# Performance work log

Hardware: AMD Instinct MI355X
Metric: run time of the kernel (lower is better)

The kernel has to match this reference:

```python
import jax, jax.numpy as jnp
import numpy as np

MAX_LEN, BATCH, EMB = 512, 32, 41
HID, UNITS = 800, 20
BOND_LENS = jnp.array([1.329, 1.459, 1.525], jnp.float32)
BOND_ANGLES = jnp.array([2.034, 2.119, 1.937], jnp.float32)
INIT_ABC = jnp.array([[0.0, 0.0, 1.0], [0.0, 1.0, 0.0], [1.0, 0.0, 0.0]], jnp.float32)


def _lstm_dir(x, w_ih, w_hh, b, reverse):
    # x: [T, B, in]; returns hidden states [T, B, H]
    T, B, _ = x.shape
    H = w_hh.shape[1]
    xs = jnp.flip(x, 0) if reverse else x
    xw = jnp.einsum('tbi,gi->tbg', xs, w_ih) + b  # precompute input projection

    def step(carry, xt):
        h, c = carry
        gates = xt + h @ w_hh.T
        i, f, g, o = jnp.split(gates, 4, axis=-1)
        c = jax.nn.sigmoid(f) * c + jax.nn.sigmoid(i) * jnp.tanh(g)
        h = jax.nn.sigmoid(o) * jnp.tanh(c)
        return (h, c), h

    init = (jnp.zeros((B, H), x.dtype), jnp.zeros((B, H), x.dtype))
    _, hs = jax.lax.scan(step, init, xw)
    return jnp.flip(hs, 0) if reverse else hs


def _bilstm_layer(x, w_ih, w_hh, b):
    # w_ih: [2, 4H, in]; w_hh: [2, 4H, H]; b: [2, 4H]
    fwd = _lstm_dir(x, w_ih[0], w_hh[0], b[0], False)
    bwd = _lstm_dir(x, w_ih[1], w_hh[1], b[1], True)
    return jnp.concatenate([fwd, bwd], axis=-1)


def _geometric_unit(coords3, triplet):
    # coords3: [3, B, 3] last three atoms; triplet: [B, 3] torsion angles
    A, Bc, C = coords3[0], coords3[1], coords3[2]
    new = []
    for i in range(3):
        Tang, R, P = BOND_ANGLES[i], BOND_LENS[i], triplet[:, i]
        D2 = jnp.stack([-R * jnp.cos(Tang) * jnp.ones_like(P),
                        R * jnp.cos(P) * jnp.sin(Tang),
                        R * jnp.sin(P) * jnp.sin(Tang)], axis=1)  # [B,3]
        BC = C - Bc
        bc = BC / jnp.linalg.norm(BC, axis=1, keepdims=True)
        AB = Bc - A
        N = jnp.cross(AB, bc)
        n = N / jnp.linalg.norm(N, axis=1, keepdims=True)
        M = jnp.stack([bc, jnp.cross(n, bc), n], axis=2)  # [B,3,3]
        D = jnp.einsum('bij,bj->bi', M, D2) + C
        A, Bc, C = Bc, C, D
        new.append(D)
    return jnp.stack([A, Bc, C]), jnp.stack(new)  # carry, [3,B,3]


def setup_inputs() -> dict:
    key = jax.random.key(0)
    ks = jax.random.split(key, 10)
    k = 1.0 / np.sqrt(HID)
    u = lambda kk, shp, lim: jax.random.uniform(kk, shp, jnp.float32, -lim, lim)
    in0, in1 = EMB + 1, 2 * HID
    return {
        'sequences': jax.random.normal(ks[0], (MAX_LEN, BATCH, EMB), jnp.float32),
        'lengths': jnp.full((BATCH,), MAX_LEN, jnp.int64 if jax.config.jax_enable_x64 else jnp.int32),
        'w_ih0': u(ks[1], (2, 4 * HID, in0), k),
        'w_hh0': u(ks[2], (2, 4 * HID, HID), k),
        'b0': u(ks[3], (2, 4 * HID), k),
        'w_ih1': u(ks[4], (2, 4 * HID, in1), k),
        'w_hh1': u(ks[5], (2, 4 * HID, HID), k),
        'b1': u(ks[6], (2, 4 * HID), k),
        'lin_w': u(ks[7], (UNITS, 2 * HID), 1.0 / np.sqrt(2 * HID)),
        'lin_b': u(ks[8], (UNITS,), 1.0 / np.sqrt(2 * HID)),
        'alphabet': jax.random.uniform(ks[9], (UNITS, 3), jnp.float32, -3.14, 3.14),
    }


def reference(sequences, lengths, w_ih0, w_hh0, b0, w_ih1, w_hh1, b1, lin_w, lin_b, alphabet):
    T, B, _ = sequences.shape
    abs_pos = jnp.broadcast_to(jnp.arange(T, dtype=sequences.dtype)[:, None, None], (T, B, 1))
    x = jnp.concatenate([sequences, abs_pos], axis=2)  # [T, B, EMB+1]
    # 2-layer bidirectional LSTM (all lengths == max_len -> packing is identity)
    h = _bilstm_layer(x, w_ih0, w_hh0, b0)
    h = _bilstm_layer(h, w_ih1, w_hh1, b1)  # [T, B, 2H]
    # linear -> softmax over alphabet, trig angle decode
    soft = jax.nn.softmax(h @ lin_w.T + lin_b, axis=2)  # [T, B, UNITS]
    sine = soft @ jnp.sin(alphabet)   # [T, B, 3]
    cosine = soft @ jnp.cos(alphabet)
    out = jnp.arctan2(sine, cosine)   # torsion angle triplets
    # sequential geometric coordinate recurrence over timesteps 1..T-1
    init = jnp.broadcast_to(INIT_ABC[:, None, :], (3, B, 3))
    _, new_coords = jax.lax.scan(_geometric_unit, init, out[1:])  # [T-1, 3, B, 3]
    pred_coords = jnp.concatenate([init, new_coords.reshape(-1, B, 3)], axis=0)
    return pred_coords  # [3 + 3*(T-1), B, 3]
```

## Files before the change

### kernel.cpp

```cpp
#include <hip/hip_runtime.h>
#include <math.h>

#define T_LEN 512
#define NB    32
#define EMB_  41
#define IN0_  42
#define HID_  800
#define G4_   3200
#define IN1_  1600
#define NU    20
#define NCH   100

typedef unsigned short u16;
typedef unsigned int   u32;
typedef unsigned long long u64;
typedef __attribute__((ext_vector_type(8))) short short8;
typedef __attribute__((ext_vector_type(4))) float f32x4;

__device__ __forceinline__ float bf2f(u16 v) {
    union { u32 u; float f; } c; c.u = ((u32)v) << 16; return c.f;
}
__device__ __forceinline__ u16 f2bf(float f) {
    union { float f; u32 u; } c; c.f = f;
    u32 r = (c.u + 0x7fffu + ((c.u >> 16) & 1u)) >> 16;
    return (u16)r;
}
__device__ __forceinline__ short cvt_hl(float v, int hl) {
    u16 hi = f2bf(v);
    return hl ? (short)f2bf(v - bf2f(hi)) : (short)hi;
}
__device__ __forceinline__ f32x4 mfma16(short8 a, short8 b, f32x4 c) {
    return __builtin_amdgcn_mfma_f32_16x16x32_bf16(a, b, c, 0, 0, 0);
}
__device__ __forceinline__ void astore(u64* p, u64 v) {
    __hip_atomic_store(p, v, __ATOMIC_RELAXED, __HIP_MEMORY_SCOPE_AGENT);
}
__device__ __forceinline__ int afload(const int* p) {
    return __hip_atomic_load(p, __ATOMIC_RELAXED, __HIP_MEMORY_SCOPE_AGENT);
}
__device__ __forceinline__ void afstore(int* p, int v) {
    __hip_atomic_store(p, v, __ATOMIC_RELAXED, __HIP_MEMORY_SCOPE_AGENT);
}


__global__ __launch_bounds__(256, 1)
void lstm0_persist(const float* __restrict__ seq, const float* __restrict__ wih0,
                   const float* __restrict__ whh0, const float* __restrict__ bias,
                   u16* __restrict__ h0f, int* __restrict__ flags)
{
    __shared__ __align__(16) float part[2048];
    __shared__ __align__(16) u16 stageB[25600];
    __shared__ __align__(16) float w0l[32*48];
    __shared__ __align__(16) float xsl[32*48];
    __shared__ u16 hpk[NB*8];
    const int tid = threadIdx.x;
    const int d = blockIdx.x / NCH, ch = blockIdx.x % NCH;
    const int w = tid >> 6, l = tid & 63;
    const int p = w & 1, hl = w >> 1;
    int* myflags = flags + d*128;

    short8 wreg[25];
    {
        const int m = l & 15, g = p*2 + (m>>3), j = ch*8 + (m&7);
        const float* base = whh0 + ((size_t)(d*G4_ + g*HID_ + j))*HID_ + (l>>4)*8;
#pragma unroll
        for (int kc = 0; kc < 25; ++kc) {
            float4 f0 = *(const float4*)(base + kc*32);
            float4 f1 = *(const float4*)(base + kc*32 + 4);
            short8 v;
            v[0]=cvt_hl(f0.x,hl); v[1]=cvt_hl(f0.y,hl); v[2]=cvt_hl(f0.z,hl); v[3]=cvt_hl(f0.w,hl);
            v[4]=cvt_hl(f1.x,hl); v[5]=cvt_hl(f1.y,hl); v[6]=cvt_hl(f1.z,hl); v[7]=cvt_hl(f1.w,hl);
            wreg[kc] = v;
        }
    }
    for (int idx = tid; idx < 32*EMB_; idx += 256) {
        int r = idx / EMB_, k = idx % EMB_;
        int ju_ = r >> 2, g = r & 3;
        w0l[r*48 + k] = wih0[((size_t)(d*G4_ + g*HID_ + ch*8 + ju_))*IN0_ + k];
    }
    const int ju = tid >> 5, b = tid & 31;
    const int j = ch*8 + ju;
    const int nt = b >> 4, n = b & 15;
    float biasr[4], wpos[4];
#pragma unroll
    for (int g = 0; g < 4; ++g) {
        biasr[g] = bias[d*G4_ + g*HID_ + j];
        wpos[g]  = wih0[((size_t)(d*G4_ + g*HID_ + j))*IN0_ + EMB_];
    }
    float creg = 0.f;
    __syncthreads();

    for (int s = 0; s < T_LEN; ++s) {
        const int t = d ? (T_LEN-1-s) : s;

        for (int idx = tid; idx < 32*EMB_; idx += 256)
            xsl[(idx/EMB_)*48 + idx%EMB_] = seq[(size_t)t*(NB*EMB_) + idx];

        if (s > 0 && tid < NCH)
            while (afload(myflags + tid) < s) __builtin_amdgcn_s_sleep(1);
        __syncthreads();

        if (s == 0) {
#pragma unroll
            for (int q = 0; q < 25; ++q) ((u64*)stageB)[tid + q*256] = 0ull;
        } else {
            const int tprev = d ? (T_LEN - s) : (s - 1);
            const u64* src = (const u64*)(h0f + (size_t)tprev*51200) + d*6400;
            u64 tmp[25];
#pragma unroll
            for (int q = 0; q < 25; ++q) tmp[q] = src[tid + q*256];
#pragma unroll
            for (int q = 0; q < 25; ++q) ((u64*)stageB)[tid + q*256] = tmp[q];
        }
        __syncthreads();

        f32x4 acc0 = {0.f,0.f,0.f,0.f}, acc1 = {0.f,0.f,0.f,0.f};
#pragma unroll 5
        for (int kc = 0; kc < 25; ++kc) {
            short8 b0 = *(const short8*)(stageB + kc*1024 + l*8);
            short8 b1 = *(const short8*)(stageB + kc*1024 + 512 + l*8);
            acc0 = mfma16(wreg[kc], b0, acc0);
            acc1 = mfma16(wreg[kc], b1, acc1);
        }
        {
            const int mrow = (l>>4)*4, nn = l & 15;
#pragma unroll
            for (int r = 0; r < 4; ++r) {
                part[(((p*2+hl)*2 + 0)*16 + mrow + r)*16 + nn] = acc0[r];
                part[(((p*2+hl)*2 + 1)*16 + mrow + r)*16 + nn] = acc1[r];
            }
        }
        __syncthreads();

        float dot0 = 0.f, dot1 = 0.f, dot2 = 0.f, dot3 = 0.f;
        {
            const float* wr = &w0l[ju*4*48];
            const float* xr = &xsl[b*48];
#pragma unroll
            for (int k4 = 0; k4 < 40; k4 += 4) {
                float4 xk = *(const float4*)(xr + k4);
                float4 w0 = *(const float4*)(wr + 0*48 + k4);
                float4 w1 = *(const float4*)(wr + 1*48 + k4);
                float4 w2 = *(const float4*)(wr + 2*48 + k4);
                float4 w3 = *(const float4*)(wr + 3*48 + k4);
                dot0 += w0.x*xk.x + w0.y*xk.y + w0.z*xk.z + w0.w*xk.w;
                dot1 += w1.x*xk.x + w1.y*xk.y + w1.z*xk.z + w1.w*xk.w;
                dot2 += w2.x*xk.x + w2.y*xk.y + w2.z*xk.z + w2.w*xk.w;
                dot3 += w3.x*xk.x + w3.y*xk.y + w3.z*xk.z + w3.w*xk.w;
            }
            float xk = xr[40];
            dot0 += wr[0*48+40]*xk; dot1 += wr[1*48+40]*xk;
            dot2 += wr[2*48+40]*xk; dot3 += wr[3*48+40]*xk;
        }
        float v[4] = {dot0, dot1, dot2, dot3};
#pragma unroll
        for (int g = 0; g < 4; ++g) {
            const int pp = g >> 1, m = (g & 1)*8 + ju;
            v[g] += part[(((pp*2+0)*2 + nt)*16 + m)*16 + n]
                  + part[(((pp*2+1)*2 + nt)*16 + m)*16 + n]
                  + biasr[g] + (float)t * wpos[g];
        }
        float ig = 1.f/(1.f + expf(-v[0]));
        float fg = 1.f/(1.f + expf(-v[1]));
        float gg = tanhf(v[2]);
        float og = 1.f/(1.f + expf(-v[3]));
        creg = fg * creg + ig * gg;
        hpk[b*8 + ju] = f2bf(og * tanhf(creg));
        __syncthreads();

        if (tid < 64) {
            const int bb = tid >> 1, half = tid & 1;
            const u16* hp = &hpk[bb*8 + half*4];
            u64 pk = (u64)hp[0] | ((u64)hp[1]<<16) | ((u64)hp[2]<<32) | ((u64)hp[3]<<48);
            const int ntb = bb >> 4, llb = ((ch&3)<<4) | (bb&15);
            const int xoff = ((d*25 + (ch>>2))*2 + ntb)*128 + llb*2 + half;
            astore((u64*)(h0f + (size_t)t*51200) + xoff, pk);
        }
        __syncthreads();
        if (tid == 0) afstore(myflags + ch, s+1);
    }
}

__global__ __launch_bounds__(256, 1)
void lstm1_persist(const float* __restrict__ wih1, const float* __restrict__ whh1,
                   const float* __restrict__ bias, const float* __restrict__ lin_w,
                   const u16* __restrict__ h0f, u16* __restrict__ h1f,
                   int* __restrict__ flags, float* __restrict__ logits)
{
    __shared__ __align__(16) u16 wihL[2*50*512];
    __shared__ __align__(16) u16 stageB[25600];
    __shared__ __align__(16) float part[2048];
    __shared__ u16 hpk[NB*8];
    const int tid = threadIdx.x;
    const int d = blockIdx.x / NCH, ch = blockIdx.x % NCH;
    const int w = tid >> 6, l = tid & 63;
    const int p = w & 1, hl = w >> 1;
    int* myflags = flags + d*128;

    short8 wreg[25];
    {
        const int m = l & 15, g = p*2 + (m>>3), j = ch*8 + (m&7);
        const float* base = whh1 + ((size_t)(d*G4_ + g*HID_ + j))*HID_ + (l>>4)*8;
#pragma unroll
        for (int kc = 0; kc < 25; ++kc) {
            float4 f0 = *(const float4*)(base + kc*32);
            float4 f1 = *(const float4*)(base + kc*32 + 4);
            short8 v;
            v[0]=cvt_hl(f0.x,hl); v[1]=cvt_hl(f0.y,hl); v[2]=cvt_hl(f0.z,hl); v[3]=cvt_hl(f0.w,hl);
            v[4]=cvt_hl(f1.x,hl); v[5]=cvt_hl(f1.y,hl); v[6]=cvt_hl(f1.z,hl); v[7]=cvt_hl(f1.w,hl);
            wreg[kc] = v;
        }
    }
    for (int o = tid; o < 6400; o += 256) {
        int pp = o / 3200, r = o % 3200, kc = r >> 6, ll = r & 63;
        int m = ll & 15, g = pp*2 + (m>>3), jj = ch*8 + (m&7);
        const float* base = wih1 + ((size_t)(d*G4_ + g*HID_ + jj))*IN1_ + kc*32 + (ll>>4)*8;
        float4 f0 = *(const float4*)base;
        float4 f1 = *(const float4*)(base + 4);
        short8 v;
        v[0]=(short)f2bf(f0.x); v[1]=(short)f2bf(f0.y); v[2]=(short)f2bf(f0.z); v[3]=(short)f2bf(f0.w);
        v[4]=(short)f2bf(f1.x); v[5]=(short)f2bf(f1.y); v[6]=(short)f2bf(f1.z); v[7]=(short)f2bf(f1.w);
        *(short8*)&wihL[o*8] = v;
    }
    const int ol = tid >> 5, ln = tid & 31;
    const int lo = ch*7 + ol;
    const bool lown = (ol < 7) && (lo < NB*NU);
    int lofs = 0;
    float wlin[25];
    if (lown) {
        const int bb = lo / NU, uu = lo % NU;
        lofs = (bb >> 4)*512 + ((((ln >> 3) << 4) | (bb & 15)))*8 + (ln & 7);
        const float* wrow = lin_w + (size_t)uu*IN1_ + d*HID_ + ln;
#pragma unroll
        for (int i = 0; i < 25; ++i) wlin[i] = wrow[i*32];
    }
    const int ju = tid >> 5, b = tid & 31;
    const int j = ch*8 + ju;
    const int nt = b >> 4, n = b & 15;
    float biasr[4];
#pragma unroll
    for (int g = 0; g < 4; ++g) biasr[g] = bias[d*G4_ + g*HID_ + j];
    float creg = 0.f;
    __syncthreads();

    for (int s = 0; s < T_LEN; ++s) {
        const int t = d ? (T_LEN-1-s) : s;

        f32x4 acc0 = {0.f,0.f,0.f,0.f}, acc1 = {0.f,0.f,0.f,0.f};
        {
            const u16* xb = h0f + (size_t)t*51200;
#pragma unroll 5
            for (int kc = 0; kc < 25; ++kc) {
                const int idx = hl*25 + kc;
                short8 a  = *(const short8*)&wihL[(p*50 + idx)*512 + l*8];
                short8 b0 = *(const short8*)(xb + idx*1024 + l*8);
                short8 b1 = *(const short8*)(xb + idx*1024 + 512 + l*8);
                acc0 = mfma16(a, b0, acc0);
                acc1 = mfma16(a, b1, acc1);
            }
        }

        if (s > 0 && tid < NCH)
            while (afload(myflags + tid) < s) __builtin_amdgcn_s_sleep(1);
        __syncthreads();

        if (s == 0) {
#pragma unroll
            for (int q = 0; q < 25; ++q) ((u64*)stageB)[tid + q*256] = 0ull;
        } else {
            const int tprev = d ? (T_LEN - s) : (s - 1);
            const u64* src = (const u64*)(h1f + (size_t)tprev*51200) + d*6400;
            u64 tmp[25];
#pragma unroll
            for (int q = 0; q < 25; ++q) tmp[q] = src[tid + q*256];
#pragma unroll
            for (int q = 0; q < 25; ++q) ((u64*)stageB)[tid + q*256] = tmp[q];
        }
        __syncthreads();

#pragma unroll 5
        for (int kc = 0; kc < 25; ++kc) {
            short8 b0 = *(const short8*)(stageB + kc*1024 + l*8);
            short8 b1 = *(const short8*)(stageB + kc*1024 + 512 + l*8);
            acc0 = mfma16(wreg[kc], b0, acc0);
            acc1 = mfma16(wreg[kc], b1, acc1);
        }
        {
            const int mrow = (l>>4)*4, nn = l & 15;
#pragma unroll
            for (int r = 0; r < 4; ++r) {
                part[(((p*2+hl)*2 + 0)*16 + mrow + r)*16 + nn] = acc0[r];
                part[(((p*2+hl)*2 + 1)*16 + mrow + r)*16 + nn] = acc1[r];
            }
        }
        __syncthreads();

        float v[4];
#pragma unroll
        for (int g = 0; g < 4; ++g) {
            const int pp = g >> 1, m = (g & 1)*8 + ju;
            v[g] = part[(((pp*2+0)*2 + nt)*16 + m)*16 + n]
                 + part[(((pp*2+1)*2 + nt)*16 + m)*16 + n] + biasr[g];
        }
        float ig = 1.f/(1.f + expf(-v[0]));
        float fg = 1.f/(1.f + expf(-v[1]));
        float gg = tanhf(v[2]);
        float og = 1.f/(1.f + expf(-v[3]));
        creg = fg * creg + ig * gg;
        float hn = og * tanhf(creg);
        hpk[b*8 + ju] = f2bf(hn);
        __syncthreads();

        if (tid < 64) {
            const int bb = tid >> 1, half = tid & 1;
            const u16* hp = &hpk[bb*8 + half*4];
            u64 pk = (u64)hp[0] | ((u64)hp[1]<<16) | ((u64)hp[2]<<32) | ((u64)hp[3]<<48);
            const int ntb = bb >> 4, llb = ((ch&3)<<4) | (bb&15);
            const int xoff = ((d*25 + (ch>>2))*2 + ntb)*128 + llb*2 + half;
            astore((u64*)(h1f + (size_t)t*51200) + xoff, pk);
        }
        __syncthreads();
        if (tid == 0) afstore(myflags + ch, s+1);

        if (s > 0 && lown) {
            float sum = 0.f;
#pragma unroll
            for (int i = 0; i < 25; ++i)
                sum += bf2f(stageB[i*1024 + lofs]) * wlin[i];
#pragma unroll
            for (int off2 = 16; off2; off2 >>= 1) sum += __shfl_down(sum, off2, 32);
            if (ln == 0) {
                const int tprev = d ? (T_LEN - s) : (s - 1);
                logits[((size_t)d*T_LEN + tprev)*640 + lo] = sum;
            }
        }
    }
    if (tid < NCH)
        while (afload(myflags + tid) < T_LEN) __builtin_amdgcn_s_sleep(1);
    __syncthreads();
    {
        const int tlast = d ? 0 : (T_LEN - 1);
        const u64* src = (const u64*)(h1f + (size_t)tlast*51200) + d*6400;
        u64 tmp[25];
#pragma unroll
        for (int q = 0; q < 25; ++q) tmp[q] = src[tid + q*256];
#pragma unroll
        for (int q = 0; q < 25; ++q) ((u64*)stageB)[tid + q*256] = tmp[q];
    }
    __syncthreads();
    if (lown) {
        float sum = 0.f;
#pragma unroll
        for (int i = 0; i < 25; ++i)
            sum += bf2f(stageB[i*1024 + lofs]) * wlin[i];
#pragma unroll
        for (int off2 = 16; off2; off2 >>= 1) sum += __shfl_down(sum, off2, 32);
        if (ln == 0) {
            const int tprev = d ? 0 : (T_LEN - 1);
            logits[((size_t)d*T_LEN + tprev)*640 + lo] = sum;
        }
    }
}

__global__ __launch_bounds__(256)
void epilogue(const float* __restrict__ logits, const float* __restrict__ lin_b,
              const float* __restrict__ alphabet, float* __restrict__ cs)
{
    __shared__ float sa[NU*3], ca[NU*3], lb[NU];
    const int tid = threadIdx.x;
    if (tid < NU*3) { float al = alphabet[tid]; sa[tid] = sinf(al); ca[tid] = cosf(al); }
    if (tid < NU) lb[tid] = lin_b[tid];
    __syncthreads();
    const int row = blockIdx.x*256 + tid;
    if (row >= T_LEN*NB) return;
    const int t = row >> 5, b = row & 31;
    float lg[NU];
    float m = -1e30f;
#pragma unroll 4
    for (int u = 0; u < NU; ++u) {
        lg[u] = lb[u] + logits[(size_t)t*640 + b*NU + u]
                      + logits[((size_t)T_LEN + t)*640 + b*NU + u];
        m = fmaxf(m, lg[u]);
    }
    float ssum = 0.f;
#pragma unroll 4
    for (int u = 0; u < NU; ++u) { lg[u] = expf(lg[u] - m); ssum += lg[u]; }
    float inv = 1.f / ssum;
#pragma unroll
    for (int i = 0; i < 3; ++i) {
        float sv = 0.f, cv = 0.f;
#pragma unroll 4
        for (int u = 0; u < NU; ++u) {
            float sw = lg[u] * inv;
            sv += sw * sa[u*3 + i];
            cv += sw * ca[u*3 + i];
        }
        float rinv = rsqrtf(fmaxf(sv*sv + cv*cv, 1e-30f));
        *(float2*)(cs + ((size_t)row*3 + i)*2) = make_float2(cv*rinv, sv*rinv);
    }
}

__global__ __launch_bounds__(64)
void geometry(const float* __restrict__ cs, float* __restrict__ out)
{
    const int b = threadIdx.x;
    if (b >= NB) return;
    const float blen[3] = {1.329f, 1.459f, 1.525f};
    const float bang[3] = {2.034f, 2.119f, 1.937f};
    float sT[3], cT[3];
#pragma unroll
    for (int i = 0; i < 3; ++i) { sT[i] = sinf(bang[i]); cT[i] = cosf(bang[i]); }

    float Ax=0.f,Ay=0.f,Az=1.f, Bx=0.f,By=1.f,Bz=0.f, Cx=1.f,Cy=0.f,Cz=0.f;
    out[(0*NB + b)*3 + 0] = 0.f; out[(0*NB + b)*3 + 1] = 0.f; out[(0*NB + b)*3 + 2] = 1.f;
    out[(1*NB + b)*3 + 0] = 0.f; out[(1*NB + b)*3 + 1] = 1.f; out[(1*NB + b)*3 + 2] = 0.f;
    out[(2*NB + b)*3 + 0] = 1.f; out[(2*NB + b)*3 + 1] = 0.f; out[(2*NB + b)*3 + 2] = 0.f;

    for (int t = 1; t < T_LEN; ++t) {
        float2 pc[3];
#pragma unroll
        for (int i = 0; i < 3; ++i)
            pc[i] = *(const float2*)(cs + (((size_t)t*NB + b)*3 + i)*2);
#pragma unroll
        for (int i = 0; i < 3; ++i) {
            float R = blen[i];
            float d2x = -R*cT[i], d2y = R*pc[i].x*sT[i], d2z = R*pc[i].y*sT[i];
            float bcx = Cx-Bx, bcy = Cy-By, bcz = Cz-Bz;
            float inv = rsqrtf(bcx*bcx + bcy*bcy + bcz*bcz);
            bcx *= inv; bcy *= inv; bcz *= inv;
            float abx = Bx-Ax, aby = By-Ay, abz = Bz-Az;
            float nx = aby*bcz - abz*bcy;
            float ny = abz*bcx - abx*bcz;
            float nz = abx*bcy - aby*bcx;
            inv = rsqrtf(fmaxf(nx*nx + ny*ny + nz*nz, 1e-30f));
            nx *= inv; ny *= inv; nz *= inv;
            float mx = ny*bcz - nz*bcy;
            float my = nz*bcx - nx*bcz;
            float mz = nx*bcy - ny*bcx;
            float Dx = bcx*d2x + mx*d2y + nx*d2z + Cx;
            float Dy = bcy*d2x + my*d2y + ny*d2z + Cy;
            float Dz = bcz*d2x + mz*d2y + nz*d2z + Cz;
            Ax=Bx; Ay=By; Az=Bz; Bx=Cx; By=Cy; Bz=Cz; Cx=Dx; Cy=Dy; Cz=Dz;
            const int r = 3 + (t-1)*3 + i;
            out[((size_t)r*NB + b)*3 + 0] = Dx;
            out[((size_t)r*NB + b)*3 + 1] = Dy;
            out[((size_t)r*NB + b)*3 + 2] = Dz;
        }
    }
}

extern "C" void kernel_launch(void* const* d_in, const int* in_sizes, int n_in,
                              void* d_out, int out_size, void* d_ws, size_t ws_size,
                              hipStream_t stream)
{
    (void)in_sizes; (void)n_in; (void)out_size; (void)ws_size;
    const float* seq   = (const float*)d_in[0];
    const float* w_ih0 = (const float*)d_in[2];
    const float* w_hh0 = (const float*)d_in[3];
    const float* b0    = (const float*)d_in[4];
    const float* w_ih1 = (const float*)d_in[5];
    const float* w_hh1 = (const float*)d_in[6];
    const float* b1    = (const float*)d_in[7];
    const float* lin_w = (const float*)d_in[8];
    const float* lin_b = (const float*)d_in[9];
    const float* alpha = (const float*)d_in[10];

    char* ws = (char*)d_ws;
    size_t off = 0;
    u16* h0f   = (u16*)(ws + off); off += 52428800ull;
    u16* h1f   = (u16*)(ws + off); off += 52428800ull;
    int* flagsL0 = (int*)(ws + off); off += 1024ull;
    int* flagsL1 = (int*)(ws + off); off += 1024ull;
    float* logits = (float*)(ws + off); off += 2621440ull;
    float* cs = (float*)(ws + off); off += 393216ull;

    hipMemsetAsync(flagsL0, 0, 2048, stream);

    lstm0_persist<<<dim3(2*NCH), dim3(256), 0, stream>>>(seq, w_ih0, w_hh0, b0, h0f, flagsL0);

    lstm1_persist<<<dim3(2*NCH), dim3(256), 0, stream>>>(w_ih1, w_hh1, b1, lin_w, h0f, h1f,
                                                         flagsL1, logits);

    epilogue<<<dim3(64), dim3(256), 0, stream>>>(logits, lin_b, alpha, cs);
    geometry<<<dim3(1), dim3(64), 0, stream>>>(cs, (float*)d_out);
}
```

Before: 9.387 ms.

## Replace per-block flag polling with per-step arrival counters and per-wave stores

Each persistent LSTM kernel now has every wave atomically increment a per-timestep arrival counter after writing its own bf16 hidden values, and all threads spin on that single counter reaching 400. This replaces the earlier scheme of 100 threads polling 100 per-block flags, and it removes the LDS staging of h and two block-wide barriers per step. The x staging buffer is double-buffered so the barrier before the wait can be dropped, and the layer-1 logit projection now reads h from global memory instead of LDS. The risks are heavier atomic traffic on one hot counter address, and memory-ordering correctness that depends on relaxed atomics plus an explicit vmcnt wait.

```diff
diff --git a/kernel.cpp b/kernel.cpp
--- a/kernel.cpp
+++ b/kernel.cpp
@@ -10,6 +10,7 @@
 #define IN1_  1600
 #define NU    20
 #define NCH   100
+#define ARR_TGT (4*NCH)
 
 typedef unsigned short u16;
 typedef unsigned int   u32;
@@ -32,32 +33,31 @@
 __device__ __forceinline__ f32x4 mfma16(short8 a, short8 b, f32x4 c) {
     return __builtin_amdgcn_mfma_f32_16x16x32_bf16(a, b, c, 0, 0, 0);
 }
-__device__ __forceinline__ void astore(u64* p, u64 v) {
+__device__ __forceinline__ void astore32(u32* p, u32 v) {
     __hip_atomic_store(p, v, __ATOMIC_RELAXED, __HIP_MEMORY_SCOPE_AGENT);
 }
 __device__ __forceinline__ int afload(const int* p) {
     return __hip_atomic_load(p, __ATOMIC_RELAXED, __HIP_MEMORY_SCOPE_AGENT);
 }
-__device__ __forceinline__ void afstore(int* p, int v) {
-    __hip_atomic_store(p, v, __ATOMIC_RELAXED, __HIP_MEMORY_SCOPE_AGENT);
+__device__ __forceinline__ void aadd(int* p) {
+    __hip_atomic_fetch_add(p, 1, __ATOMIC_RELAXED, __HIP_MEMORY_SCOPE_AGENT);
 }
 
 
 __global__ __launch_bounds__(256, 1)
 void lstm0_persist(const float* __restrict__ seq, const float* __restrict__ wih0,
                    const float* __restrict__ whh0, const float* __restrict__ bias,
-                   u16* __restrict__ h0f, int* __restrict__ flags)
+                   u16* __restrict__ h0f, int* __restrict__ arr)
 {
     __shared__ __align__(16) float part[2048];
     __shared__ __align__(16) u16 stageB[25600];
     __shared__ __align__(16) float w0l[32*48];
-    __shared__ __align__(16) float xsl[32*48];
-    __shared__ u16 hpk[NB*8];
+    __shared__ __align__(16) float xsl[2][32*48];
     const int tid = threadIdx.x;
     const int d = blockIdx.x / NCH, ch = blockIdx.x % NCH;
     const int w = tid >> 6, l = tid & 63;
     const int p = w & 1, hl = w >> 1;
-    int* myflags = flags + d*128;
+    int* myarr = arr + d*512;
 
     short8 wreg[25];
     {
@@ -94,11 +94,10 @@
         const int t = d ? (T_LEN-1-s) : s;
 
         for (int idx = tid; idx < 32*EMB_; idx += 256)
-            xsl[(idx/EMB_)*48 + idx%EMB_] = seq[(size_t)t*(NB*EMB_) + idx];
-
-        if (s > 0 && tid < NCH)
-            while (afload(myflags + tid) < s) __builtin_amdgcn_s_sleep(1);
-        __syncthreads();
+            xsl[s&1][(idx/EMB_)*48 + idx%EMB_] = seq[(size_t)t*(NB*EMB_) + idx];
+
+        if (s > 0)
+            while (afload(myarr + (s-1)) < ARR_TGT) __builtin_amdgcn_s_sleep(1);
 
         if (s == 0) {
 #pragma unroll
@@ -135,7 +134,7 @@
         float dot0 = 0.f, dot1 = 0.f, dot2 = 0.f, dot3 = 0.f;
         {
             const float* wr = &w0l[ju*4*48];
-            const float* xr = &xsl[b*48];
+            const float* xr = &xsl[s&1][b*48];
 #pragma unroll
             for (int k4 = 0; k4 < 40; k4 += 4) {
                 float4 xk = *(const float4*)(xr + k4);
@@ -165,19 +164,18 @@
         float gg = tanhf(v[2]);
         float og = 1.f/(1.f + expf(-v[3]));
         creg = fg * creg + ig * gg;
-        hpk[b*8 + ju] = f2bf(og * tanhf(creg));
-        __syncthreads();
-
-        if (tid < 64) {
-            const int bb = tid >> 1, half = tid & 1;
-            const u16* hp = &hpk[bb*8 + half*4];
-            u64 pk = (u64)hp[0] | ((u64)hp[1]<<16) | ((u64)hp[2]<<32) | ((u64)hp[3]<<48);
-            const int ntb = bb >> 4, llb = ((ch&3)<<4) | (bb&15);
-            const int xoff = ((d*25 + (ch>>2))*2 + ntb)*128 + llb*2 + half;
-            astore((u64*)(h0f + (size_t)t*51200) + xoff, pk);
-        }
-        __syncthreads();
-        if (tid == 0) afstore(myflags + ch, s+1);
+        float hval = og * tanhf(creg);
+
+        u32 hv = (u32)f2bf(hval);
+        u32 ov = (u32)__shfl((int)hv, l | 32);
+        if (l < 32) {
+            const int ntb = b >> 4, llb = ((ch&3)<<4) | (b&15);
+            const int half = w >> 1;
+            const u32 xoff = (u32)(((d*25 + (ch>>2))*2 + ntb)*128 + llb*2 + half);
+            astore32((u32*)(h0f + (size_t)t*51200) + xoff*2 + (w&1), hv | (ov<<16));
+        }
+        asm volatile("s_waitcnt vmcnt(0)" ::: "memory");
+        if (l == 0) aadd(myarr + s);
     }
 }
 
@@ -185,17 +183,16 @@
 void lstm1_persist(const float* __restrict__ wih1, const float* __restrict__ whh1,
                    const float* __restrict__ bias, const float* __restrict__ lin_w,
                    const u16* __restrict__ h0f, u16* __restrict__ h1f,
-                   int* __restrict__ flags, float* __restrict__ logits)
+                   int* __restrict__ arr, float* __restrict__ logits)
 {
     __shared__ __align__(16) u16 wihL[2*50*512];
     __shared__ __align__(16) u16 stageB[25600];
     __shared__ __align__(16) float part[2048];
-    __shared__ u16 hpk[NB*8];
     const int tid = threadIdx.x;
     const int d = blockIdx.x / NCH, ch = blockIdx.x % NCH;
     const int w = tid >> 6, l = tid & 63;
     const int p = w & 1, hl = w >> 1;
-    int* myflags = flags + d*128;
+    int* myarr = arr + d*512;
 
     short8 wreg[25];
     {
@@ -260,9 +257,8 @@
             }
         }
 
-        if (s > 0 && tid < NCH)
-            while (afload(myflags + tid) < s) __builtin_amdgcn_s_sleep(1);
-        __syncthreads();
+        if (s > 0)
+            while (afload(myarr + (s-1)) < ARR_TGT) __builtin_amdgcn_s_sleep(1);
 
         if (s == 0) {
 #pragma unroll
@@ -307,58 +303,44 @@
         float gg = tanhf(v[2]);
         float og = 1.f/(1.f + expf(-v[3]));
         creg = fg * creg + ig * gg;
-        float hn = og * tanhf(creg);
-        hpk[b*8 + ju] = f2bf(hn);
-        __syncthreads();
-
-        if (tid < 64) {
-            const int bb = tid >> 1, half = tid & 1;
-            const u16* hp = &hpk[bb*8 + half*4];
-            u64 pk = (u64)hp[0] | ((u64)hp[1]<<16) | ((u64)hp[2]<<32) | ((u64)hp[3]<<48);
-            const int ntb = bb >> 4, llb = ((ch&3)<<4) | (bb&15);
-            const int xoff = ((d*25 + (ch>>2))*2 + ntb)*128 + llb*2 + half;
-            astore((u64*)(h1f + (size_t)t*51200) + xoff, pk);
-        }
-        __syncthreads();
-        if (tid == 0) afstore(myflags + ch, s+1);
+        float hval = og * tanhf(creg);
+
+        u32 hv = (u32)f2bf(hval);
+        u32 ov = (u32)__shfl((int)hv, l | 32);
+        if (l < 32) {
+            const int ntb = b >> 4, llb = ((ch&3)<<4) | (b&15);
+            const int half = w >> 1;
+            const u32 xoff = (u32)(((d*25 + (ch>>2))*2 + ntb)*128 + llb*2 + half);
+            astore32((u32*)(h1f + (size_t)t*51200) + xoff*2 + (w&1), hv | (ov<<16));
+        }
+        asm volatile("s_waitcnt vmcnt(0)" ::: "memory");
+        if (l == 0) aadd(myarr + s);
 
         if (s > 0 && lown) {
+            const int tprev = d ? (T_LEN - s) : (s - 1);
+            const u16* hb = h1f + (size_t)tprev*51200 + d*25600;
             float sum = 0.f;
 #pragma unroll
             for (int i = 0; i < 25; ++i)
-                sum += bf2f(stageB[i*1024 + lofs]) * wlin[i];
+                sum += bf2f(hb[i*1024 + lofs]) * wlin[i];
 #pragma unroll
             for (int off2 = 16; off2; off2 >>= 1) sum += __shfl_down(sum, off2, 32);
-            if (ln == 0) {
-                const int tprev = d ? (T_LEN - s) : (s - 1);
+            if (ln == 0)
                 logits[((size_t)d*T_LEN + tprev)*640 + lo] = sum;
-            }
-        }
-    }
-    if (tid < NCH)
-        while (afload(myflags + tid) < T_LEN) __builtin_amdgcn_s_sleep(1);
-    __syncthreads();
-    {
+        }
+    }
+    while (afload(myarr + (T_LEN-1)) < ARR_TGT) __builtin_amdgcn_s_sleep(1);
+    if (lown) {
         const int tlast = d ? 0 : (T_LEN - 1);
-        const u64* src = (const u64*)(h1f + (size_t)tlast*51200) + d*6400;
-        u64 tmp[25];
-#pragma unroll
-        for (int q = 0; q < 25; ++q) tmp[q] = src[tid + q*256];
-#pragma unroll
-        for (int q = 0; q < 25; ++q) ((u64*)stageB)[tid + q*256] = tmp[q];
-    }
-    __syncthreads();
-    if (lown) {
+        const u16* hb = h1f + (size_t)tlast*51200 + d*25600;
         float sum = 0.f;
 #pragma unroll
         for (int i = 0; i < 25; ++i)
-            sum += bf2f(stageB[i*1024 + lofs]) * wlin[i];
+            sum += bf2f(hb[i*1024 + lofs]) * wlin[i];
 #pragma unroll
         for (int off2 = 16; off2; off2 >>= 1) sum += __shfl_down(sum, off2, 32);
-        if (ln == 0) {
-            const int tprev = d ? 0 : (T_LEN - 1);
-            logits[((size_t)d*T_LEN + tprev)*640 + lo] = sum;
-        }
+        if (ln == 0)
+            logits[((size_t)d*T_LEN + tlast)*640 + lo] = sum;
     }
 }
 
@@ -469,17 +451,17 @@
     size_t off = 0;
     u16* h0f   = (u16*)(ws + off); off += 52428800ull;
     u16* h1f   = (u16*)(ws + off); off += 52428800ull;
-    int* flagsL0 = (int*)(ws + off); off += 1024ull;
-    int* flagsL1 = (int*)(ws + off); off += 1024ull;
+    int* arrL0 = (int*)(ws + off); off += 4096ull;
+    int* arrL1 = (int*)(ws + off); off += 4096ull;
     float* logits = (float*)(ws + off); off += 2621440ull;
     float* cs = (float*)(ws + off); off += 393216ull;
 
-    hipMemsetAsync(flagsL0, 0, 2048, stream);
-
-    lstm0_persist<<<dim3(2*NCH), dim3(256), 0, stream>>>(seq, w_ih0, w_hh0, b0, h0f, flagsL0);
+    hipMemsetAsync(arrL0, 0, 8192, stream);
+
+    lstm0_persist<<<dim3(2*NCH), dim3(256), 0, stream>>>(seq, w_ih0, w_hh0, b0, h0f, arrL0);
 
     lstm1_persist<<<dim3(2*NCH), dim3(256), 0, stream>>>(w_ih1, w_hh1, b1, lin_w, h0f, h1f,
-                                                         flagsL1, logits);
+                                                         arrL1, logits);
 
     epilogue<<<dim3(64), dim3(256), 0, stream>>>(logits, lin_b, alpha, cs);
     geometry<<<dim3(1), dim3(64), 0, stream>>>(cs, (float*)d_out);
```

Measured after the change: 11.44 ms. 1.22x slower.

## Halve layer-0 LSTM blocks, each handling two hidden-unit chunks

Applied to the files above, without the earlier changes.

Layer 0's persistent kernel now launches 100 blocks instead of 200, and each block owns 16 hidden units instead of 8. The recurrent weights for both chunks stay in registers, and per step each block issues twice the MFMAs on the same staged h tile. This halves the number of blocks each step's flag wait must poll, and halves the redundant copy of the full hidden state into shared memory. In exchange each block does more serial compute per step and uses more registers for the doubled weight arrays. The per-step input tile is also double-buffered in shared memory.

```diff
diff --git a/kernel.cpp b/kernel.cpp
--- a/kernel.cpp
+++ b/kernel.cpp
@@ -9,6 +9,7 @@
 #define G4_   3200
 #define IN1_  1600
 #define NU    20
+#define NCH0  50
 #define NCH   100
 
 typedef unsigned short u16;
@@ -48,55 +49,62 @@
                    const float* __restrict__ whh0, const float* __restrict__ bias,
                    u16* __restrict__ h0f, int* __restrict__ flags)
 {
-    __shared__ __align__(16) float part[2048];
+    __shared__ __align__(16) float part[4096];
     __shared__ __align__(16) u16 stageB[25600];
-    __shared__ __align__(16) float w0l[32*48];
-    __shared__ __align__(16) float xsl[32*48];
-    __shared__ u16 hpk[NB*8];
+    __shared__ __align__(16) float w0l[64*48];
+    __shared__ __align__(16) float xsl[2][32*48];
+    __shared__ u16 hpk[2][NB*8];
     const int tid = threadIdx.x;
-    const int d = blockIdx.x / NCH, ch = blockIdx.x % NCH;
+    const int d = blockIdx.x / NCH0, ch = blockIdx.x % NCH0;
     const int w = tid >> 6, l = tid & 63;
     const int p = w & 1, hl = w >> 1;
     int* myflags = flags + d*128;
 
-    short8 wreg[25];
+    short8 wreg[2][25];
     {
-        const int m = l & 15, g = p*2 + (m>>3), j = ch*8 + (m&7);
-        const float* base = whh0 + ((size_t)(d*G4_ + g*HID_ + j))*HID_ + (l>>4)*8;
-#pragma unroll
-        for (int kc = 0; kc < 25; ++kc) {
-            float4 f0 = *(const float4*)(base + kc*32);
-            float4 f1 = *(const float4*)(base + kc*32 + 4);
-            short8 v;
-            v[0]=cvt_hl(f0.x,hl); v[1]=cvt_hl(f0.y,hl); v[2]=cvt_hl(f0.z,hl); v[3]=cvt_hl(f0.w,hl);
-            v[4]=cvt_hl(f1.x,hl); v[5]=cvt_hl(f1.y,hl); v[6]=cvt_hl(f1.z,hl); v[7]=cvt_hl(f1.w,hl);
-            wreg[kc] = v;
-        }
-    }
-    for (int idx = tid; idx < 32*EMB_; idx += 256) {
+        const int m = l & 15, g = p*2 + (m>>3);
+#pragma unroll
+        for (int T = 0; T < 2; ++T) {
+            const int j = (ch*2 + T)*8 + (m&7);
+            const float* base = whh0 + ((size_t)(d*G4_ + g*HID_ + j))*HID_ + (l>>4)*8;
+#pragma unroll
+            for (int kc = 0; kc < 25; ++kc) {
+                float4 f0 = *(const float4*)(base + kc*32);
+                float4 f1 = *(const float4*)(base + kc*32 + 4);
+                short8 v;
+                v[0]=cvt_hl(f0.x,hl); v[1]=cvt_hl(f0.y,hl); v[2]=cvt_hl(f0.z,hl); v[3]=cvt_hl(f0.w,hl);
+                v[4]=cvt_hl(f1.x,hl); v[5]=cvt_hl(f1.y,hl); v[6]=cvt_hl(f1.z,hl); v[7]=cvt_hl(f1.w,hl);
+                wreg[T][kc] = v;
+            }
+        }
+    }
+    for (int idx = tid; idx < 64*EMB_; idx += 256) {
         int r = idx / EMB_, k = idx % EMB_;
         int ju_ = r >> 2, g = r & 3;
-        w0l[r*48 + k] = wih0[((size_t)(d*G4_ + g*HID_ + ch*8 + ju_))*IN0_ + k];
+        w0l[r*48 + k] = wih0[((size_t)(d*G4_ + g*HID_ + ch*16 + ju_))*IN0_ + k];
     }
     const int ju = tid >> 5, b = tid & 31;
-    const int j = ch*8 + ju;
     const int nt = b >> 4, n = b & 15;
-    float biasr[4], wpos[4];
-#pragma unroll
-    for (int g = 0; g < 4; ++g) {
-        biasr[g] = bias[d*G4_ + g*HID_ + j];
-        wpos[g]  = wih0[((size_t)(d*G4_ + g*HID_ + j))*IN0_ + EMB_];
-    }
-    float creg = 0.f;
+    float biasr[2][4], wpos[2][4];
+#pragma unroll
+    for (int T = 0; T < 2; ++T) {
+        const int j = ch*16 + T*8 + ju;
+#pragma unroll
+        for (int g = 0; g < 4; ++g) {
+            biasr[T][g] = bias[d*G4_ + g*HID_ + j];
+            wpos[T][g]  = wih0[((size_t)(d*G4_ + g*HID_ + j))*IN0_ + EMB_];
+        }
+    }
+    float creg[2] = {0.f, 0.f};
     __syncthreads();
 
     for (int s = 0; s < T_LEN; ++s) {
         const int t = d ? (T_LEN-1-s) : s;
 
         for (int idx = tid; idx < 32*EMB_; idx += 256)
-            xsl[(idx/EMB_)*48 + idx%EMB_] = seq[(size_t)t*(NB*EMB_) + idx];
-
-        if (s > 0 && tid < NCH)
+            xsl[s&1][(idx/EMB_)*48 + idx%EMB_] = seq[(size_t)t*(NB*EMB_) + idx];
+
+        if (s > 0 && tid < NCH0)
             while (afload(myflags + tid) < s) __builtin_amdgcn_s_sleep(1);
         __syncthreads();
 
@@ -114,28 +122,34 @@
         }
         __syncthreads();
 
-        f32x4 acc0 = {0.f,0.f,0.f,0.f}, acc1 = {0.f,0.f,0.f,0.f};
-#pragma unroll 5
+        f32x4 a00 = {0.f,0.f,0.f,0.f}, a01 = {0.f,0.f,0.f,0.f};
+        f32x4 a10 = {0.f,0.f,0.f,0.f}, a11 = {0.f,0.f,0.f,0.f};
+#pragma unroll
         for (int kc = 0; kc < 25; ++kc) {
             short8 b0 = *(const short8*)(stageB + kc*1024 + l*8);
             short8 b1 = *(const short8*)(stageB + kc*1024 + 512 + l*8);
-            acc0 = mfma16(wreg[kc], b0, acc0);
-            acc1 = mfma16(wreg[kc], b1, acc1);
+            a00 = mfma16(wreg[0][kc], b0, a00);
+            a01 = mfma16(wreg[0][kc], b1, a01);
+            a10 = mfma16(wreg[1][kc], b0, a10);
+            a11 = mfma16(wreg[1][kc], b1, a11);
         }
         {
             const int mrow = (l>>4)*4, nn = l & 15;
 #pragma unroll
             for (int r = 0; r < 4; ++r) {
-                part[(((p*2+hl)*2 + 0)*16 + mrow + r)*16 + nn] = acc0[r];
-                part[(((p*2+hl)*2 + 1)*16 + mrow + r)*16 + nn] = acc1[r];
-            }
-        }
-        __syncthreads();
-
-        float dot0 = 0.f, dot1 = 0.f, dot2 = 0.f, dot3 = 0.f;
-        {
-            const float* wr = &w0l[ju*4*48];
-            const float* xr = &xsl[b*48];
+                part[((0*8 + (p*2+hl)*2 + 0)*16 + mrow + r)*16 + nn] = a00[r];
+                part[((0*8 + (p*2+hl)*2 + 1)*16 + mrow + r)*16 + nn] = a01[r];
+                part[((1*8 + (p*2+hl)*2 + 0)*16 + mrow + r)*16 + nn] = a10[r];
+                part[((1*8 + (p*2+hl)*2 + 1)*16 + mrow + r)*16 + nn] = a11[r];
+            }
+        }
+        __syncthreads();
+
+#pragma unroll
+        for (int T = 0; T < 2; ++T) {
+            float dot0 = 0.f, dot1 = 0.f, dot2 = 0.f, dot3 = 0.f;
+            const float* wr = &w0l[(T*8 + ju)*4*48];
+            const float* xr = &xsl[s&1][b*48];
 #pragma unroll
             for (int k4 = 0; k4 < 40; k4 += 4) {
                 float4 xk = *(const float4*)(xr + k4);
@@ -151,29 +165,31 @@
             float xk = xr[40];
             dot0 += wr[0*48+40]*xk; dot1 += wr[1*48+40]*xk;
             dot2 += wr[2*48+40]*xk; dot3 += wr[3*48+40]*xk;
-        }
-        float v[4] = {dot0, dot1, dot2, dot3};
-#pragma unroll
-        for (int g = 0; g < 4; ++g) {
-            const int pp = g >> 1, m = (g & 1)*8 + ju;
-            v[g] += part[(((pp*2+0)*2 + nt)*16 + m)*16 + n]
-                  + part[(((pp*2+1)*2 + nt)*16 + m)*16 + n]
-                  + biasr[g] + (float)t * wpos[g];
-        }
-        float ig = 1.f/(1.f + expf(-v[0]));
-        float fg = 1.f/(1.f + expf(-v[1]));
-        float gg = tanhf(v[2]);
-        float og = 1.f/(1.f + expf(-v[3]));
-        creg = fg * creg + ig * gg;
-        hpk[b*8 + ju] = f2bf(og * tanhf(creg));
-        __syncthreads();
-
-        if (tid < 64) {
-            const int bb = tid >> 1, half = tid & 1;
-            const u16* hp = &hpk[bb*8 + half*4];
+            float v[4] = {dot0, dot1, dot2, dot3};
+#pragma unroll
+            for (int g = 0; g < 4; ++g) {
+                const int pp = g >> 1, m = (g & 1)*8 + ju;
+                v[g] += part[((T*8 + (pp*2+0)*2 + nt)*16 + m)*16 + n]
+                      + part[((T*8 + (pp*2+1)*2 + nt)*16 + m)*16 + n]
+                      + biasr[T][g] + (float)t * wpos[T][g];
+            }
+            float ig = 1.f/(1.f + expf(-v[0]));
+            float fg = 1.f/(1.f + expf(-v[1]));
+            float gg = tanhf(v[2]);
+            float og = 1.f/(1.f + expf(-v[3]));
+            creg[T] = fg * creg[T] + ig * gg;
+            hpk[T][b*8 + ju] = f2bf(og * tanhf(creg[T]));
+        }
+        __syncthreads();
+
+        if (tid < 128) {
+            const int T = tid >> 6, tl = tid & 63;
+            const int bb = tl >> 1, half = tl & 1;
+            const u16* hp = &hpk[T][bb*8 + half*4];
             u64 pk = (u64)hp[0] | ((u64)hp[1]<<16) | ((u64)hp[2]<<32) | ((u64)hp[3]<<48);
-            const int ntb = bb >> 4, llb = ((ch&3)<<4) | (bb&15);
-            const int xoff = ((d*25 + (ch>>2))*2 + ntb)*128 + llb*2 + half;
+            const int ch2 = ch*2 + T;
+            const int ntb = bb >> 4, llb = ((ch2&3)<<4) | (bb&15);
+            const int xoff = ((d*25 + (ch2>>2))*2 + ntb)*128 + llb*2 + half;
             astore((u64*)(h0f + (size_t)t*51200) + xoff, pk);
         }
         __syncthreads();
@@ -476,7 +492,7 @@
 
     hipMemsetAsync(flagsL0, 0, 2048, stream);
 
-    lstm0_persist<<<dim3(2*NCH), dim3(256), 0, stream>>>(seq, w_ih0, w_hh0, b0, h0f, flagsL0);
+    lstm0_persist<<<dim3(2*NCH0), dim3(256), 0, stream>>>(seq, w_ih0, w_hh0, b0, h0f, flagsL0);
 
     lstm1_persist<<<dim3(2*NCH), dim3(256), 0, stream>>>(w_ih1, w_hh1, b1, lin_w, h0f, h1f,
                                                          flagsL1, logits);
```

Result: no change. 9.321 ms (-0.7%).
